# Kernel tuning notes

Measured on AMD Instinct MI355X. Metric: run time of the kernel, lower is better.

The kernel has to match this reference:

```python
import jax, jax.numpy as jnp
import numpy as np

H = 256; S = 64; AN = 16; D = 8; HH = 8; WW = 8; T = 32; N = 64; NV = 32
HG = 2 + 3 * H  # GRU hidden = sum(parser_sections) = 1 + 1 + 3*H


def _gru(x, w_ih, w_hh, b_ih, b_hh):
    """torch-style GRU over leading axis; x: [L, N, Hin] -> [L, N, HG]."""
    def step(h, xt):
        gi = xt @ w_ih.T + b_ih
        gh = h @ w_hh.T + b_hh
        ir, iz, inn = jnp.split(gi, 3, axis=-1)
        hr, hz, hn = jnp.split(gh, 3, axis=-1)
        r = jax.nn.sigmoid(ir + hr)
        z = jax.nn.sigmoid(iz + hz)
        n = jnp.tanh(inn + r * hn)
        h2 = (1 - z) * n + z * h
        return h2, h2
    h0 = jnp.zeros((x.shape[1], w_hh.shape[1]), x.dtype)
    _, ys = jax.lax.scan(step, h0, x)
    return ys


def _cos(e, m):  # e [N,H], m [N,S,H] -> [N,S]; matches F.cosine_similarity eps=1e-8
    num = jnp.einsum('nh,nsh->ns', e, m)
    den = jnp.linalg.norm(e, axis=-1)[:, None] * jnp.linalg.norm(m, axis=-1)
    return num / jnp.maximum(den, 1e-8)


def _l1norm(x):  # F.normalize(x, p=1, dim=-1)
    return x / jnp.maximum(jnp.abs(x).sum(-1, keepdims=True), 1e-12)


def setup_inputs():
    key = jax.random.key(0)
    ks = jax.random.split(key, 16)
    sc = lambda k, shape, fan: jax.random.normal(k, shape, jnp.float32) / np.float32(np.sqrt(fan))
    return dict(
        base=jax.random.normal(ks[0], (T, N, D, HH, WW), jnp.float32),
        interactable=(jax.random.uniform(ks[1], (T, N, AN - 5)) < 0.5).astype(jnp.float32),
        rnn_hxs=jnp.zeros((1, N, 1 + AN + 1 + H + S), jnp.float32),
        emb=sc(ks[2], (NV, H), 1.0),
        gru_w_ih=sc(ks[3], (3 * HG, H), H),
        gru_w_hh=sc(ks[4], (3 * HG, HG), HG),
        gru_b_ih=jnp.zeros((3 * HG,), jnp.float32),
        gru_b_hh=jnp.zeros((3 * HG,), jnp.float32),
        conv0_w=sc(ks[5], (H, D * H), D * H),
        conv0_b=jnp.zeros((H,), jnp.float32),
        convs_w=sc(ks[6], (2, H, H), H),
        convs_b=jnp.zeros((2, H), jnp.float32),
        lin_w=sc(ks[7], (H, H * HH * WW), H * HH * WW),
        lin_b=jnp.zeros((H,), jnp.float32),
        psi_w=sc(ks[8], (H, H * AN), H * AN),
        psi_b=jnp.zeros((H,), jnp.float32),
        actor_w=sc(ks[9], (AN, H), H),
        actor_b=jnp.zeros((AN,), jnp.float32),
        critic_w=sc(ks[10], (1, H), H),
        critic_b=jnp.zeros((1,), jnp.float32),
        subtasks=jax.random.randint(ks[11], (N, S), 0, NV),
        actions=jax.random.randint(ks[12], (T, N), 0, AN),
    )


def reference(base, interactable, rnn_hxs, emb, gru_w_ih, gru_w_hh, gru_b_ih, gru_b_hh,
              conv0_w, conv0_b, convs_w, convs_b, lin_w, lin_b, psi_w, psi_b,
              actor_w, actor_b, critic_w, critic_b, subtasks, actions):
    # --- parser: GRU over the subtask token sequence ---
    rnn_in = emb[subtasks].transpose(1, 0, 2)                                    # [S, N, H]
    X = _gru(rnn_in, gru_w_ih, gru_w_hh, gru_b_ih, gru_b_hh).transpose(1, 0, 2)  # [N, S, HG]
    c, p0 = X[..., 0], X[..., 1]                                                 # [N, S]
    M = X[..., 2:2 + H]
    Mm = X[..., 2 + H:2 + 2 * H]
    Mp = X[..., 2 + 2 * H:]
    hx = rnn_hxs[0]
    new_ep = jnp.all(rnn_hxs == 0, axis=-1)[0]                                   # [N]
    p_init = jnp.where(new_ep[:, None], p0, hx[:, 1 + AN + 1 + H:])

    def f_net(base_t, r):
        n = base_t.shape[0]
        # outer product [N,H,d,h,w] -> [N, H*d, h, w], then 1x1 convs
        x = (base_t[:, None] * r[:, :, None, None, None]).reshape(n, H * D, HH, WW)
        x = jax.nn.relu(jnp.einsum('nchw,oc->nohw', x, conv0_w) + conv0_b[None, :, None, None])
        for i in range(convs_w.shape[0]):
            x = jax.nn.relu(jnp.einsum('nchw,oc->nohw', x, convs_w[i]) + convs_b[i][None, :, None, None])
        return jax.nn.relu(x.reshape(n, -1) @ lin_w.T + lin_b)

    def step(p, xs):
        base_t, inter_t, a_t = xs
        ps = jax.nn.softmax(p, axis=-1)
        r = jnp.einsum('ns,nsh->nh', ps, M)                                      # memory read
        s = f_net(base_t, r)
        dprobs = jax.nn.softmax(s @ actor_w.T + actor_b, axis=-1)
        nonzero = jnp.pad(inter_t, ((0, 0), (5, 0)), constant_values=1.0)        # [N, AN]
        probs = dprobs * nonzero
        deficit = 1.0 - probs.sum(-1, keepdims=True)
        probs = probs + _l1norm(nonzero) * deficit
        probs = _l1norm(jnp.clip(probs, 0.0, 1.0))
        a_oh = jax.nn.one_hot(a_t, AN, dtype=s.dtype)
        e = (s[:, :, None] * a_oh[:, None, :]).reshape(s.shape[0], H * AN) @ psi_w.T + psi_b
        p_new = ps + c * _cos(e, Mp) - c * _cos(e, Mm)                           # memory write
        v = s @ critic_w.T + critic_b
        out = jnp.concatenate([a_t[:, None].astype(s.dtype), probs, v, s, p_new], axis=-1)
        return p_new, out

    _, hx_out = jax.lax.scan(step, p_init, (base, interactable, actions))        # [T, N, 338]
    return hx_out, hx_out[-1:]
```

## Files before the change

### kernel.cpp

```cpp
#include <hip/hip_runtime.h>
#include <math.h>

constexpr int cH  = 256;
constexpr int cS  = 64;
constexpr int cAN = 16;
constexpr int cD  = 8;
constexpr int cT  = 32;
constexpr int cN  = 64;
constexpr int cHG = 770;
constexpr int cG3 = 2310;
constexpr int cOW = 338;
constexpr int XLD = 800;
constexpr int GLD = 832;
constexpr int MLD = 2496;
constexpr int PROW = 2560;

__global__ __launch_bounds__(256) void k_gitab(const float* __restrict__ emb,
                                               const float* __restrict__ w_ih,
                                               const float* __restrict__ b_ih,
                                               float* __restrict__ gitp) {
  int v = blockIdx.y;
  int j = blockIdx.x * 256 + threadIdx.x;
  __shared__ float es[cH];
  es[threadIdx.x] = emb[v * cH + threadIdx.x];
  __syncthreads();
  if (j < cG3) {
    float acc = b_ih[j];
    const float* wr = w_ih + (size_t)j * cH;
    #pragma unroll 8
    for (int h = 0; h < cH; ++h) acc += wr[h] * es[h];
    int g = j / cHG, kk = j - g * cHG;
    gitp[(size_t)v * MLD + g * GLD + kk] = acc;
  }
}

__global__ __launch_bounds__(256) void k_wpad(const float* __restrict__ whh,
                                              float* __restrict__ wpadG) {
  int idx = blockIdx.x * 256 + threadIdx.x;
  if (idx < PROW * XLD) {
    int row = idx / XLD, col = idx - row * XLD;
    int g = row / GLD, k = row - g * GLD;
    wpadG[idx] = (g < 3 && k < cHG && col < cHG)
                     ? whh[(size_t)(g * cHG + k) * cHG + col] : 0.f;
  }
}

__global__ __launch_bounds__(256) void k_psiperm(const float* __restrict__ psi_w,
                                                 float* __restrict__ psip) {
  int idx = blockIdx.x * 256 + threadIdx.x;
  int a = idx >> 16, h = (idx >> 8) & 255, o = idx & 255;
  psip[idx] = psi_w[((size_t)o * cH + h) * cAN + a];
}

__global__ __launch_bounds__(256) void k_gru_gemm(const float* __restrict__ wpadG,
                                                  const float* __restrict__ X,
                                                  float* __restrict__ part, int s) {
  int tid = threadIdx.x;
  int tile = blockIdx.x % 40;
  int ks   = blockIdx.x / 40;
  int g = tile / 13, kt = tile - g * 13;
  int cbase = (ks <= 2) ? ks * 13 : 38;
  int ccnt  = (ks < 2) ? 13 : 12;
  int kbase = cbase * 16;
  int csz = ccnt * 16;

  __shared__ float Bst[208][68];
  __shared__ float As[2][16][68];

  const float* bsrc = wpadG + ((size_t)(g * GLD + kt * 64)) * XLD + kbase;
  for (int i = tid; i < 64 * 208; i += 256) {
    int jl = i / 208, k2l = i - jl * 208;
    if (k2l < csz) Bst[k2l][jl] = bsrc[(size_t)jl * XLD + k2l];
  }

  int tm = tid & 15, tj = tid >> 4;
  int lrow = tid >> 2, lcol = (tid & 3) * 4;
  __syncthreads();

  float acc[4][4] = {};
  const float* Xp = X + ((size_t)lrow * cS + (s - 1)) * XLD + kbase;
  float4 av = *(const float4*)(Xp + lcol);
  for (int c = 0; c < ccnt; ++c) {
    int buf = c & 1;
    As[buf][lcol + 0][lrow] = av.x;
    As[buf][lcol + 1][lrow] = av.y;
    As[buf][lcol + 2][lrow] = av.z;
    As[buf][lcol + 3][lrow] = av.w;
    __syncthreads();
    if (c + 1 < ccnt) av = *(const float4*)(Xp + (c + 1) * 16 + lcol);
    #pragma unroll
    for (int kk = 0; kk < 16; ++kk) {
      float4 a4 = *(const float4*)&As[buf][kk][tm * 4];
      float4 b4 = *(const float4*)&Bst[c * 16 + kk][tj * 4];
      acc[0][0] += a4.x * b4.x; acc[0][1] += a4.x * b4.y; acc[0][2] += a4.x * b4.z; acc[0][3] += a4.x * b4.w;
      acc[1][0] += a4.y * b4.x; acc[1][1] += a4.y * b4.y; acc[1][2] += a4.y * b4.z; acc[1][3] += a4.y * b4.w;
      acc[2][0] += a4.z * b4.x; acc[2][1] += a4.z * b4.y; acc[2][2] += a4.z * b4.z; acc[2][3] += a4.z * b4.w;
      acc[3][0] += a4.w * b4.x; acc[3][1] += a4.w * b4.y; acc[3][2] += a4.w * b4.z; acc[3][3] += a4.w * b4.w;
    }
    __syncthreads();
  }
  float* pw = part + (size_t)ks * (64 * PROW) + (size_t)(g * GLD + kt * 64);
  #pragma unroll
  for (int i = 0; i < 4; ++i) {
    *(float4*)(pw + (size_t)(tm * 4 + i) * PROW + tj * 4) =
        make_float4(acc[i][0], acc[i][1], acc[i][2], acc[i][3]);
  }
}

__global__ __launch_bounds__(256) void k_gru_gate(const float* __restrict__ part,
                                                  const float* __restrict__ bhh,
                                                  const float* __restrict__ gitp,
                                                  const int* __restrict__ subtasks,
                                                  float* __restrict__ X, int s) {
  int kq = blockIdx.x, m = blockIdx.y, tid = threadIdx.x;
  if (tid >= 200) return;
  int k = kq * 200 + tid;
  float* xrow = X + ((size_t)m * cS + s) * XLD;
  if (k >= cHG) { if (k < XLD) xrow[k] = 0.f; return; }
  float accr = 0.f, accz = 0.f, accn = 0.f;
  if (s > 0) {
    const float* pm = part + (size_t)m * PROW;
    #pragma unroll
    for (int q = 0; q < 4; ++q) {
      const float* pq = pm + (size_t)q * (64 * PROW);
      accr += pq[k];
      accz += pq[GLD + k];
      accn += pq[2 * GLD + k];
    }
  }
  int v = subtasks[m * cS + s];
  const float* git = gitp + (size_t)v * MLD;
  float rg = 1.f / (1.f + expf(-(git[k]           + accr + bhh[k])));
  float zg = 1.f / (1.f + expf(-(git[GLD + k]     + accz + bhh[cHG + k])));
  float ng = tanhf(git[2 * GLD + k] + rg * (accn + bhh[2 * cHG + k]));
  float hp = (s > 0) ? X[((size_t)m * cS + (s - 1)) * XLD + k] : 0.f;
  xrow[k] = (1.f - zg) * ng + zg * hp;
}

__global__ __launch_bounds__(256) void k_pinit(const float* __restrict__ hxs,
                                               const float* __restrict__ X,
                                               float* __restrict__ psb,
                                               float* __restrict__ r,
                                               float* __restrict__ nMp,
                                               float* __restrict__ nMm) {
  int n = blockIdx.x, tid = threadIdx.x;
  __shared__ int anynz;
  __shared__ float pss[cS];
  __shared__ float mx, sm;
  if (tid == 0) anynz = 0;
  __syncthreads();
  int nz = (hxs[n * cOW + tid] != 0.f) ? 1 : 0;
  if (tid + 256 < cOW) nz |= (hxs[n * cOW + tid + 256] != 0.f) ? 1 : 0;
  if (nz) anynz = 1;
  __syncthreads();
  bool newep = (anynz == 0);
  if (tid < cS) {
    const float* xr = X + ((size_t)n * cS + tid) * XLD;
    float p0 = xr[1];
    float pv = newep ? p0 : hxs[n * cOW + 1 + cAN + 1 + cH + tid];
    pss[tid] = pv;
    float sp = 0.f, smn = 0.f;
    for (int h = 0; h < cH; ++h) {
      float vp = xr[2 + 2 * cH + h]; sp += vp * vp;
      float vm = xr[2 + cH + h];     smn += vm * vm;
    }
    nMp[n * cS + tid] = sqrtf(sp);
    nMm[n * cS + tid] = sqrtf(smn);
  }
  __syncthreads();
  if (tid == 0) { float m = pss[0]; for (int i = 1; i < cS; ++i) m = fmaxf(m, pss[i]); mx = m; }
  __syncthreads();
  if (tid < cS) pss[tid] = expf(pss[tid] - mx);
  __syncthreads();
  if (tid == 0) { float s = 0.f; for (int i = 0; i < cS; ++i) s += pss[i]; sm = s; }
  __syncthreads();
  if (tid < cS) { pss[tid] /= sm; psb[n * cS + tid] = pss[tid]; }
  __syncthreads();
  float acc = 0.f;
  for (int s2 = 0; s2 < cS; ++s2)
    acc += pss[s2] * X[((size_t)n * cS + s2) * XLD + 2 + tid];
  r[n * cH + tid] = acc;
}

__global__ __launch_bounds__(256) void k_front(const float* __restrict__ r,
                                               const float* __restrict__ base,
                                               const float* __restrict__ cw,
                                               const float* __restrict__ cb,
                                               float* __restrict__ x1T, int t) {
  int o = blockIdx.x, tid = threadIdx.x;
  __shared__ float rsQ[64][65][4];
  __shared__ float w0s[64][9];

  #pragma unroll
  for (int it = 0; it < 16; ++it) {
    int flat4 = it * 256 + tid;
    int n = flat4 >> 6, hq = flat4 & 63;
    float4 v = *(const float4*)(r + n * cH + hq * 4);
    *(float4*)&rsQ[hq][n][0] = v;
  }
  __syncthreads();

  {
    int dg = tid >> 6, n = tid & 63;
    int d0 = dg * 2;
    const float* cwo = cw + (size_t)o * (cD * cH);
    float acc0 = 0.f, acc1 = 0.f;
    #pragma unroll 4
    for (int hq = 0; hq < 64; ++hq) {
      float4 rv = *(const float4*)&rsQ[hq][n][0];
      #pragma unroll
      for (int j = 0; j < 4; ++j) {
        float2 w = *(const float2*)(cwo + (hq * 4 + j) * 8 + d0);
        float rvj = ((const float*)&rv)[j];
        acc0 += w.x * rvj;
        acc1 += w.y * rvj;
      }
    }
    w0s[n][d0]     = acc0;
    w0s[n][d0 + 1] = acc1;
  }
  __syncthreads();

  {
    int q = tid >> 6, n = tid & 63;
    float w0[8];
    #pragma unroll
    for (int d = 0; d < 8; ++d) w0[d] = w0s[n][d];
    float bias = cb[o];
    const float4* b4 = (const float4*)(base + ((size_t)(t * cN + n) * cD) * 64);
    float* dst = x1T + (size_t)o * 4096 + n * 64 + q * 16;
    #pragma unroll
    for (int k = 0; k < 4; ++k) {
      float4 acc = make_float4(bias, bias, bias, bias);
      #pragma unroll
      for (int d = 0; d < 8; ++d) {
        float4 bv = b4[d * 16 + q * 4 + k];
        acc.x += w0[d] * bv.x; acc.y += w0[d] * bv.y;
        acc.z += w0[d] * bv.z; acc.w += w0[d] * bv.w;
      }
      acc.x = fmaxf(acc.x, 0.f); acc.y = fmaxf(acc.y, 0.f);
      acc.z = fmaxf(acc.z, 0.f); acc.w = fmaxf(acc.w, 0.f);
      *(float4*)(dst + k * 4) = acc;
    }
  }
}

__global__ __launch_bounds__(256) void k_gemmT(const float* __restrict__ AT,
                                               const float* __restrict__ W,
                                               const float* __restrict__ bias,
                                               float* __restrict__ C, int mode) {
  int nb = blockIdx.x, mb = blockIdx.y, tid = threadIdx.x;
  int tm = tid & 15, tj = tid >> 4;
  __shared__ float As[16][68];
  __shared__ float Bs[16][68];
  float acc[4][4] = {{0.f}};
  int lrow = tid >> 2, lcol = (tid & 3) * 4;
  int kr = tid >> 4, mc4 = (tid & 15) * 4;
  for (int kc = 0; kc < cH; kc += 16) {
    float4 av = *(const float4*)(AT + (size_t)(kc + kr) * 4096 + mb * 64 + mc4);
    float4 wv = *(const float4*)(W + (size_t)(nb * 64 + lrow) * cH + kc + lcol);
    *(float4*)&As[kr][mc4] = av;
    Bs[lcol][lrow] = wv.x; Bs[lcol + 1][lrow] = wv.y; Bs[lcol + 2][lrow] = wv.z; Bs[lcol + 3][lrow] = wv.w;
    __syncthreads();
    #pragma unroll
    for (int kk = 0; kk < 16; ++kk) {
      float4 a4 = *(const float4*)&As[kk][tm * 4];
      float4 b4 = *(const float4*)&Bs[kk][tj * 4];
      acc[0][0] += a4.x * b4.x; acc[0][1] += a4.x * b4.y; acc[0][2] += a4.x * b4.z; acc[0][3] += a4.x * b4.w;
      acc[1][0] += a4.y * b4.x; acc[1][1] += a4.y * b4.y; acc[1][2] += a4.y * b4.z; acc[1][3] += a4.y * b4.w;
      acc[2][0] += a4.z * b4.x; acc[2][1] += a4.z * b4.y; acc[2][2] += a4.z * b4.z; acc[2][3] += a4.z * b4.w;
      acc[3][0] += a4.w * b4.x; acc[3][1] += a4.w * b4.y; acc[3][2] += a4.w * b4.z; acc[3][3] += a4.w * b4.w;
    }
    __syncthreads();
  }
  if (mode == 0) {
    #pragma unroll
    for (int j = 0; j < 4; ++j) {
      int o = nb * 64 + tj * 4 + j;
      float bv = bias[o];
      float4 o4;
      o4.x = fmaxf(acc[0][j] + bv, 0.f);
      o4.y = fmaxf(acc[1][j] + bv, 0.f);
      o4.z = fmaxf(acc[2][j] + bv, 0.f);
      o4.w = fmaxf(acc[3][j] + bv, 0.f);
      *(float4*)(C + (size_t)o * 4096 + mb * 64 + tm * 4) = o4;
    }
  } else {
    #pragma unroll
    for (int j = 0; j < 4; ++j) {
      int o = nb * 64 + tj * 4 + j;
      float bv = bias[o];
      float4 o4;
      o4.x = fmaxf(acc[0][j] + bv, 0.f);
      o4.y = fmaxf(acc[1][j] + bv, 0.f);
      o4.z = fmaxf(acc[2][j] + bv, 0.f);
      o4.w = fmaxf(acc[3][j] + bv, 0.f);
      *(float4*)(C + (size_t)mb * (64 * cH) + (size_t)o * 64 + tm * 4) = o4;
    }
  }
}

__global__ __launch_bounds__(256) void k_lin(const float* __restrict__ A,
                                             const float* __restrict__ W,
                                             float* __restrict__ part) {
  int nb = blockIdx.x, kcb = blockIdx.y, tid = threadIdx.x;
  int tm = tid & 15, tj = tid >> 4;
  __shared__ float As[16][68];
  __shared__ float Bs[16][68];
  float acc[4][4] = {{0.f}};
  int lrow = tid >> 2, lcol = (tid & 3) * 4;
  for (int kc = 0; kc < 256; kc += 16) {
    float4 av = *(const float4*)(A + (size_t)lrow * 16384 + kcb * 256 + kc + lcol);
    float4 wv = *(const float4*)(W + (size_t)(nb * 64 + lrow) * 16384 + kcb * 256 + kc + lcol);
    As[lcol][lrow] = av.x; As[lcol + 1][lrow] = av.y; As[lcol + 2][lrow] = av.z; As[lcol + 3][lrow] = av.w;
    Bs[lcol][lrow] = wv.x; Bs[lcol + 1][lrow] = wv.y; Bs[lcol + 2][lrow] = wv.z; Bs[lcol + 3][lrow] = wv.w;
    __syncthreads();
    #pragma unroll
    for (int kk = 0; kk < 16; ++kk) {
      float4 a4 = *(const float4*)&As[kk][tm * 4];
      float4 b4 = *(const float4*)&Bs[kk][tj * 4];
      acc[0][0] += a4.x * b4.x; acc[0][1] += a4.x * b4.y; acc[0][2] += a4.x * b4.z; acc[0][3] += a4.x * b4.w;
      acc[1][0] += a4.y * b4.x; acc[1][1] += a4.y * b4.y; acc[1][2] += a4.y * b4.z; acc[1][3] += a4.y * b4.w;
      acc[2][0] += a4.z * b4.x; acc[2][1] += a4.z * b4.y; acc[2][2] += a4.z * b4.z; acc[2][3] += a4.z * b4.w;
      acc[3][0] += a4.w * b4.x; acc[3][1] += a4.w * b4.y; acc[3][2] += a4.w * b4.z; acc[3][3] += a4.w * b4.w;
    }
    __syncthreads();
  }
  #pragma unroll
  for (int i = 0; i < 4; ++i) {
    int n = tm * 4 + i;
    float4 o4 = make_float4(acc[i][0], acc[i][1], acc[i][2], acc[i][3]);
    *(float4*)(part + ((size_t)kcb * cN + n) * cH + nb * 64 + tj * 4) = o4;
  }
}

__global__ __launch_bounds__(256) void k_tail(const float* __restrict__ part,
                                              const float* __restrict__ lin_b,
                                              const float* __restrict__ actor_w,
                                              const float* __restrict__ actor_b,
                                              const float* __restrict__ critic_w,
                                              const float* __restrict__ critic_b,
                                              const float* __restrict__ psip,
                                              const float* __restrict__ psi_b,
                                              const float* __restrict__ inter,
                                              const int* __restrict__ actions,
                                              const float* __restrict__ X,
                                              const float* __restrict__ nMp,
                                              const float* __restrict__ nMm,
                                              float* __restrict__ psb,
                                              float* __restrict__ r,
                                              float* __restrict__ out, int t) {
  int n = blockIdx.x, tid = threadIdx.x;
  __shared__ float ss[cH];
  __shared__ float es[cH];
  __shared__ float lg[cAN], dp[cAN], nzv[cAN], prb[cAN];
  __shared__ float red[256];
  __shared__ float ared[16][17];
  __shared__ float cred[2][4][64];
  __shared__ float enorm_s;
  __shared__ float pns[cS];
  __shared__ float mx2, sm2;
  float* orow = out + ((size_t)t * cN + n) * cOW;
  float acc = lin_b[tid];
  for (int kc = 0; kc < 64; ++kc) acc += part[((size_t)kc * cN + n) * cH + tid];
  float sv = fmaxf(acc, 0.f);
  ss[tid] = sv;
  orow[1 + cAN + 1 + tid] = sv;
  __syncthreads();
  {
    int a = tid & 15, hg = tid >> 4;
    float pa = 0.f;
    const float* wr = actor_w + a * cH + hg * 16;
    const float* sh = &ss[hg * 16];
    #pragma unroll
    for (int hh2 = 0; hh2 < 16; ++hh2) pa += wr[hh2] * sh[hh2];
    ared[a][hg] = pa;
  }
  __syncthreads();
  if (tid < cAN) {
    float a = actor_b[tid];
    #pragma unroll
    for (int i = 0; i < 16; ++i) a += ared[tid][i];
    lg[tid] = a;
  }
  __syncthreads();
  if (tid < cAN) {
    float m = lg[0];
    for (int i = 1; i < cAN; ++i) m = fmaxf(m, lg[i]);
    dp[tid] = expf(lg[tid] - m);
  }
  __syncthreads();
  if (tid < cAN) {
    float s = 0.f;
    for (int i = 0; i < cAN; ++i) s += dp[i];
    float dprob = dp[tid] / s;
    float nv = (tid < 5) ? 1.f : inter[((size_t)t * cN + n) * (cAN - 5) + (tid - 5)];
    nzv[tid] = nv;
    prb[tid] = dprob * nv;
  }
  __syncthreads();
  if (tid < cAN) {
    float sp = 0.f, sn = 0.f;
    for (int i = 0; i < cAN; ++i) { sp += prb[i]; sn += nzv[i]; }
    float deficit = 1.f - sp;
    float v2 = prb[tid] + (nzv[tid] / fmaxf(sn, 1e-12f)) * deficit;
    prb[tid] = fminf(fmaxf(v2, 0.f), 1.f);
  }
  __syncthreads();
  if (tid < cAN) {
    float s = 0.f;
    for (int i = 0; i < cAN; ++i) s += prb[i];
    orow[1 + tid] = prb[tid] / fmaxf(s, 1e-12f);
  }
  int at = actions[t * cN + n];
  {
    float a = psi_b[tid];
    for (int h = 0; h < cH; ++h) a += psip[((size_t)at * cH + h) * cH + tid] * ss[h];
    es[tid] = a;
    red[tid] = a * a;
  }
  __syncthreads();
  for (int st = 128; st > 0; st >>= 1) {
    if (tid < st) red[tid] += red[tid + st];
    __syncthreads();
  }
  if (tid == 0) enorm_s = sqrtf(red[0]);
  __syncthreads();
  float enorm = enorm_s;
  red[tid] = critic_w[tid] * ss[tid];
  __syncthreads();
  for (int st = 128; st > 0; st >>= 1) {
    if (tid < st) red[tid] += red[tid + st];
    __syncthreads();
  }
  if (tid == 0) {
    orow[1 + cAN] = red[0] + critic_b[0];
    orow[0] = (float)at;
  }
  {
    int s2 = tid & 63, hg = tid >> 6;
    const float* xr = X + ((size_t)n * cS + s2) * XLD;
    const float* xp = xr + 2 + 2 * cH + hg * 64;
    const float* xm = xr + 2 + cH + hg * 64;
    const float* ep = &es[hg * 64];
    float dpp = 0.f, dmm = 0.f;
    #pragma unroll 8
    for (int h2 = 0; h2 < 64; ++h2) {
      float ev = ep[h2];
      dpp += ev * xp[h2];
      dmm += ev * xm[h2];
    }
    cred[0][hg][s2] = dpp;
    cred[1][hg][s2] = dmm;
  }
  __syncthreads();
  if (tid < cS) {
    float dpp = cred[0][0][tid] + cred[0][1][tid] + cred[0][2][tid] + cred[0][3][tid];
    float dmm = cred[1][0][tid] + cred[1][1][tid] + cred[1][2][tid] + cred[1][3][tid];
    const float* xr = X + ((size_t)n * cS + tid) * XLD;
    float cP = dpp / fmaxf(enorm * nMp[n * cS + tid], 1e-8f);
    float cM = dmm / fmaxf(enorm * nMm[n * cS + tid], 1e-8f);
    float cc = xr[0];
    float pn = psb[n * cS + tid] + cc * cP - cc * cM;
    pns[tid] = pn;
    orow[1 + cAN + 1 + cH + tid] = pn;
  }
  __threadfence_block();
  __syncthreads();
  if (t == cT - 1) {
    float* orow2 = out + (size_t)cT * cN * cOW + (size_t)n * cOW;
    orow2[tid] = orow[tid];
    if (tid + 256 < cOW) orow2[tid + 256] = orow[tid + 256];
  }
  if (tid == 0) { float m2 = pns[0]; for (int i = 1; i < cS; ++i) m2 = fmaxf(m2, pns[i]); mx2 = m2; }
  __syncthreads();
  if (tid < cS) pns[tid] = expf(pns[tid] - mx2);
  __syncthreads();
  if (tid == 0) { float s2 = 0.f; for (int i = 0; i < cS; ++i) s2 += pns[i]; sm2 = s2; }
  __syncthreads();
  if (tid < cS) { pns[tid] /= sm2; psb[n * cS + tid] = pns[tid]; }
  __syncthreads();
  float acc2 = 0.f;
  for (int s2 = 0; s2 < cS; ++s2)
    acc2 += pns[s2] * X[((size_t)n * cS + s2) * XLD + 2 + tid];
  r[n * cH + tid] = acc2;
}

extern "C" void kernel_launch(void* const* d_in, const int* in_sizes, int n_in,
                              void* d_out, int out_size, void* d_ws, size_t ws_size,
                              hipStream_t stream) {
  const float* base     = (const float*)d_in[0];
  const float* inter    = (const float*)d_in[1];
  const float* hxs      = (const float*)d_in[2];
  const float* emb      = (const float*)d_in[3];
  const float* w_ih     = (const float*)d_in[4];
  const float* w_hh     = (const float*)d_in[5];
  const float* b_ih     = (const float*)d_in[6];
  const float* b_hh     = (const float*)d_in[7];
  const float* conv0_w  = (const float*)d_in[8];
  const float* conv0_b  = (const float*)d_in[9];
  const float* convs_w  = (const float*)d_in[10];
  const float* convs_b  = (const float*)d_in[11];
  const float* lin_w    = (const float*)d_in[12];
  const float* lin_b    = (const float*)d_in[13];
  const float* psi_w    = (const float*)d_in[14];
  const float* psi_b    = (const float*)d_in[15];
  const float* actor_w  = (const float*)d_in[16];
  const float* actor_b  = (const float*)d_in[17];
  const float* critic_w = (const float*)d_in[18];
  const float* critic_b = (const float*)d_in[19];
  const int*   subtasks = (const int*)d_in[20];
  const int*   actions  = (const int*)d_in[21];
  float* out = (float*)d_out;
  float* ws  = (float*)d_ws;

  float* gitp  = ws + 0;
  float* psb   = ws + 0;
  float* r     = ws + 4096;
  float* nMp   = ws + 20480;
  float* nMm   = ws + 24576;
  float* X     = ws + 79872;
  float* wpadG = ws + 3356672;
  float* psip  = ws + 3356672;
  float* x1T   = ws + 4405248;
  float* part  = x1T;
  float* partG = ws + 5404672;
  float* x2T   = ws + 5453824;
  float* x3t   = ws + 6502400;

  k_gitab<<<dim3(10, 32), 256, 0, stream>>>(emb, w_ih, b_ih, gitp);
  k_wpad<<<8000, 256, 0, stream>>>(w_hh, wpadG);
  k_gru_gate<<<dim3(4, 64), 256, 0, stream>>>(partG, b_hh, gitp, subtasks, X, 0);
  for (int s = 1; s < cS; ++s) {
    k_gru_gemm<<<160, 256, 0, stream>>>(wpadG, X, partG, s);
    k_gru_gate<<<dim3(4, 64), 256, 0, stream>>>(partG, b_hh, gitp, subtasks, X, s);
  }
  k_psiperm<<<4096, 256, 0, stream>>>(psi_w, psip);
  k_pinit<<<64, 256, 0, stream>>>(hxs, X, psb, r, nMp, nMm);
  for (int t = 0; t < cT; ++t) {
    k_front<<<256, 256, 0, stream>>>(r, base, conv0_w, conv0_b, x1T, t);
    k_gemmT<<<dim3(4, 64), 256, 0, stream>>>(x1T, convs_w, convs_b, x2T, 0);
    k_gemmT<<<dim3(4, 64), 256, 0, stream>>>(x2T, convs_w + 65536, convs_b + 256, x3t, 1);
    k_lin<<<dim3(4, 64), 256, 0, stream>>>(x3t, lin_w, part);
    k_tail<<<64, 256, 0, stream>>>(part, lin_b, actor_w, actor_b, critic_w, critic_b,
                                   psip, psi_b, inter, actions, X, nMp, nMm,
                                   psb, r, out, t);
  }
}
```

Baseline: 4.611 ms.

## Fuse conv0 output construction into first 1x1 conv GEMM via shared memory

Splits the front kernel so it only computes the per-sample reduced conv0 weights (w0r). A new kernel rebuilds the conv0 activations for one sample in shared memory from w0r and the base input, then runs the first 1x1 conv GEMM directly on them. This removes the global write and re-read of the x1T intermediate. In exchange, each of the 4 output-column blocks per sample recomputes the conv0 activations, and the kernel uses a large shared-memory footprint that limits occupancy.

```diff
diff --git a/kernel.cpp b/kernel.cpp
--- a/kernel.cpp
+++ b/kernel.cpp
@@ -182,15 +182,11 @@
   r[n * cH + tid] = acc;
 }
 
-__global__ __launch_bounds__(256) void k_front(const float* __restrict__ r,
-                                               const float* __restrict__ base,
-                                               const float* __restrict__ cw,
-                                               const float* __restrict__ cb,
-                                               float* __restrict__ x1T, int t) {
+__global__ __launch_bounds__(256) void k_front0(const float* __restrict__ r,
+                                                const float* __restrict__ cw,
+                                                float* __restrict__ w0r) {
   int o = blockIdx.x, tid = threadIdx.x;
   __shared__ float rsQ[64][65][4];
-  __shared__ float w0s[64][9];
-
   #pragma unroll
   for (int it = 0; it < 16; ++it) {
     int flat4 = it * 256 + tid;
@@ -199,49 +195,92 @@
     *(float4*)&rsQ[hq][n][0] = v;
   }
   __syncthreads();
-
+  int dg = tid >> 6, n = tid & 63;
+  int d0 = dg * 2;
+  const float* cwo = cw + (size_t)o * (cD * cH);
+  float acc0 = 0.f, acc1 = 0.f;
+  #pragma unroll 4
+  for (int hq = 0; hq < 64; ++hq) {
+    float4 rv = *(const float4*)&rsQ[hq][n][0];
+    #pragma unroll
+    for (int j = 0; j < 4; ++j) {
+      float2 w = *(const float2*)(cwo + (hq * 4 + j) * 8 + d0);
+      float rvj = ((const float*)&rv)[j];
+      acc0 += w.x * rvj;
+      acc1 += w.y * rvj;
+    }
+  }
+  w0r[(size_t)n * 2048 + o * 8 + d0]     = acc0;
+  w0r[(size_t)n * 2048 + o * 8 + d0 + 1] = acc1;
+}
+
+__global__ __launch_bounds__(256) void k_conv1f(const float* __restrict__ w0r,
+                                                const float* __restrict__ base,
+                                                const float* __restrict__ cb0,
+                                                const float* __restrict__ W1,
+                                                const float* __restrict__ b1,
+                                                float* __restrict__ y1T, int t) {
+  int b = blockIdx.x, tid = threadIdx.x;
+  int n  = (b & 7) | ((b >> 5) << 3);
+  int nb = (b >> 3) & 3;
+  __shared__ float x1s[256][68];
+  __shared__ float w0s[256][9];
+  __shared__ float bs[8][64];
+  __shared__ float Bs[16][68];
   {
-    int dg = tid >> 6, n = tid & 63;
-    int d0 = dg * 2;
-    const float* cwo = cw + (size_t)o * (cD * cH);
-    float acc0 = 0.f, acc1 = 0.f;
-    #pragma unroll 4
-    for (int hq = 0; hq < 64; ++hq) {
-      float4 rv = *(const float4*)&rsQ[hq][n][0];
+    const float* src = w0r + (size_t)n * 2048 + tid * 8;
+    float4 va = *(const float4*)(src);
+    float4 vb = *(const float4*)(src + 4);
+    *(float4*)&w0s[tid][0] = va;
+    *(float4*)&w0s[tid][4] = vb;
+    w0s[tid][8] = cb0[tid];
+  }
+  if (tid < 128) {
+    int d = tid >> 4, c4 = (tid & 15) * 4;
+    *(float4*)&bs[d][c4] =
+        *(const float4*)(base + ((size_t)(t * cN + n) * cD + d) * 64 + c4);
+  }
+  __syncthreads();
+  {
+    int wv = tid >> 6, ln = tid & 63;
+    for (int oi = 0; oi < 64; ++oi) {
+      int o = wv * 64 + oi;
+      float acc = w0s[o][8];
       #pragma unroll
-      for (int j = 0; j < 4; ++j) {
-        float2 w = *(const float2*)(cwo + (hq * 4 + j) * 8 + d0);
-        float rvj = ((const float*)&rv)[j];
-        acc0 += w.x * rvj;
-        acc1 += w.y * rvj;
-      }
-    }
-    w0s[n][d0]     = acc0;
-    w0s[n][d0 + 1] = acc1;
-  }
-  __syncthreads();
-
-  {
-    int q = tid >> 6, n = tid & 63;
-    float w0[8];
-    #pragma unroll
-    for (int d = 0; d < 8; ++d) w0[d] = w0s[n][d];
-    float bias = cb[o];
-    const float4* b4 = (const float4*)(base + ((size_t)(t * cN + n) * cD) * 64);
-    float* dst = x1T + (size_t)o * 4096 + n * 64 + q * 16;
-    #pragma unroll
-    for (int k = 0; k < 4; ++k) {
-      float4 acc = make_float4(bias, bias, bias, bias);
-      #pragma unroll
-      for (int d = 0; d < 8; ++d) {
-        float4 bv = b4[d * 16 + q * 4 + k];
-        acc.x += w0[d] * bv.x; acc.y += w0[d] * bv.y;
-        acc.z += w0[d] * bv.z; acc.w += w0[d] * bv.w;
-      }
-      acc.x = fmaxf(acc.x, 0.f); acc.y = fmaxf(acc.y, 0.f);
-      acc.z = fmaxf(acc.z, 0.f); acc.w = fmaxf(acc.w, 0.f);
-      *(float4*)(dst + k * 4) = acc;
-    }
+      for (int d = 0; d < 8; ++d) acc += w0s[o][d] * bs[d][ln];
+      x1s[o][ln] = fmaxf(acc, 0.f);
+    }
+  }
+  __syncthreads();
+  int tm = tid & 15, tj = tid >> 4;
+  int lrow = tid >> 2, lcol = (tid & 3) * 4;
+  float acc[4][4] = {{0.f}};
+  for (int kc = 0; kc < cH; kc += 16) {
+    float4 wv4 = *(const float4*)(W1 + (size_t)(nb * 64 + lrow) * cH + kc + lcol);
+    Bs[lcol][lrow] = wv4.x; Bs[lcol + 1][lrow] = wv4.y;
+    Bs[lcol + 2][lrow] = wv4.z; Bs[lcol + 3][lrow] = wv4.w;
+    __syncthreads();
+    #pragma unroll
+    for (int kk = 0; kk < 16; ++kk) {
+      float4 a4 = *(const float4*)&x1s[kc + kk][tm * 4];
+      float4 b4 = *(const float4*)&Bs[kk][tj * 4];
+      acc[0][0] += a4.x * b4.x; acc[0][1] += a4.x * b4.y; acc[0][2] += a4.x * b4.z; acc[0][3] += a4.x * b4.w;
+      acc[1][0] += a4.y * b4.x; acc[1][1] += a4.y * b4.y; acc[1][2] += a4.y * b4.z; acc[1][3] += a4.y * b4.w;
+      acc[2][0] += a4.z * b4.x; acc[2][1] += a4.z * b4.y; acc[2][2] += a4.z * b4.z; acc[2][3] += a4.z * b4.w;
+      acc[3][0] += a4.w * b4.x; acc[3][1] += a4.w * b4.y; acc[3][2] += a4.w * b4.z; acc[3][3] += a4.w * b4.w;
+    }
+    __syncthreads();
+  }
+  #pragma unroll
+  for (int j = 0; j < 4; ++j) {
+    int o = nb * 64 + tj * 4 + j;
+    float bv = b1[o];
+    float4 o4;
+    o4.x = fmaxf(acc[0][j] + bv, 0.f);
+    o4.y = fmaxf(acc[1][j] + bv, 0.f);
+    o4.z = fmaxf(acc[2][j] + bv, 0.f);
+    o4.w = fmaxf(acc[3][j] + bv, 0.f);
+    *(float4*)(y1T + (size_t)o * 4096 + n * 64 + tm * 4) = o4;
   }
 }
 
@@ -514,19 +553,20 @@
   float* out = (float*)d_out;
   float* ws  = (float*)d_ws;
 
-  float* gitp  = ws + 0;
-  float* psb   = ws + 0;
-  float* r     = ws + 4096;
-  float* nMp   = ws + 20480;
-  float* nMm   = ws + 24576;
-  float* X     = ws + 79872;
-  float* wpadG = ws + 3356672;
-  float* psip  = ws + 3356672;
-  float* x1T   = ws + 4405248;
-  float* part  = x1T;
-  float* partG = ws + 5404672;
-  float* x2T   = ws + 5453824;
-  float* x3t   = ws + 6502400;
+  float* gitp   = ws + 0;
+  float* psb    = ws + 0;
+  float* r      = ws + 4096;
+  float* nMp    = ws + 20480;
+  float* nMm    = ws + 24576;
+  float* X      = ws + 79872;
+  float* wpadG  = ws + 3356672;
+  float* psip   = ws + 3356672;
+  float* x1T    = ws + 4405248;
+  float* part   = x1T;
+  float* partG  = ws + 5404672;
+  float* x2T    = ws + 5453824;
+  float* x3t    = ws + 6502400;
+  float* w0r    = ws + 7550976;
 
   k_gitab<<<dim3(10, 32), 256, 0, stream>>>(emb, w_ih, b_ih, gitp);
   k_wpad<<<8000, 256, 0, stream>>>(w_hh, wpadG);
@@ -538,8 +578,8 @@
   k_psiperm<<<4096, 256, 0, stream>>>(psi_w, psip);
   k_pinit<<<64, 256, 0, stream>>>(hxs, X, psb, r, nMp, nMm);
   for (int t = 0; t < cT; ++t) {
-    k_front<<<256, 256, 0, stream>>>(r, base, conv0_w, conv0_b, x1T, t);
-    k_gemmT<<<dim3(4, 64), 256, 0, stream>>>(x1T, convs_w, convs_b, x2T, 0);
+    k_front0<<<256, 256, 0, stream>>>(r, conv0_w, w0r);
+    k_conv1f<<<256, 256, 0, stream>>>(w0r, base, conv0_b, convs_w, convs_b, x2T, t);
     k_gemmT<<<dim3(4, 64), 256, 0, stream>>>(x2T, convs_w + 65536, convs_b + 256, x3t, 1);
     k_lin<<<dim3(4, 64), 256, 0, stream>>>(x3t, lin_w, part);
     k_tail<<<64, 256, 0, stream>>>(part, lin_b, actor_w, actor_b, critic_w, critic_b,
```

Measured after the change: 4.447 ms, median of 2. 1.04x faster.
